# Kernel tuning notes

Measured on AMD Instinct MI355X. Metric: run time of the kernel, lower is better.

The kernel has to match this reference:

```python
import jax, jax.numpy as jnp
import numpy as np

B, L, D, H = 2, 2048, 1024, 16
DH = D // H
LN_EPS = 1e-5


def setup_inputs() -> dict:
    key = jax.random.key(0)
    ks = jax.random.split(key, 6)
    s = 1.0 / np.sqrt(D)
    return {
        "x": jax.random.normal(ks[0], (B, L, D), dtype=jnp.float32),
        "market_info": jax.random.uniform(ks[1], (B, 8), dtype=jnp.float32),
        "in_proj_w": jax.random.normal(ks[2], (3 * D, D), dtype=jnp.float32) * s,
        "in_proj_b": jnp.zeros((3 * D,), dtype=jnp.float32),
        "out_proj_w": jax.random.normal(ks[3], (D, D), dtype=jnp.float32) * s,
        "out_proj_b": jnp.zeros((D,), dtype=jnp.float32),
        "ln_gamma": jnp.ones((D,), dtype=jnp.float32),
        "ln_beta": jnp.zeros((D,), dtype=jnp.float32),
    }


def reference(x, market_info, in_proj_w, in_proj_b, out_proj_w, out_proj_b, ln_gamma, ln_beta):
    # fused QKV projection (torch nn.MultiheadAttention in_proj)
    qkv = jnp.einsum("bld,ed->ble", x, in_proj_w) + in_proj_b  # (B,L,3D)
    q, k, v = jnp.split(qkv, 3, axis=-1)
    q = q.reshape(B, L, H, DH)
    k = k.reshape(B, L, H, DH)
    v = v.reshape(B, L, H, DH)
    scale = 1.0 / jnp.sqrt(jnp.asarray(DH, dtype=x.dtype))
    scores = jnp.einsum("blhd,bmhd->bhlm", q, k) * scale  # (B,H,L,L)
    # market mask: per-batch volatility scalar added to every score
    vol = market_info[:, 0][:, None, None, None]  # (B,1,1,1)
    attn = jax.nn.softmax(scores + vol, axis=-1)
    ctx = jnp.einsum("bhlm,bmhd->blhd", attn, v).reshape(B, L, D)
    attended = jnp.einsum("bld,ed->ble", ctx, out_proj_w) + out_proj_b
    # residual + LayerNorm (dropout=0 / eval)
    y = x + attended
    mu = jnp.mean(y, axis=-1, keepdims=True)
    var = jnp.mean(jnp.square(y - mu), axis=-1, keepdims=True)
    return (y - mu) * jax.lax.rsqrt(var + LN_EPS) * ln_gamma + ln_beta
```

## Files before the change

### kernel.cpp

```cpp
#include <hip/hip_runtime.h>
#include <math.h>

#define B_  2
#define L_  2048
#define D_  1024
#define H_  16
#define DH_ 64
#define E3D 3072
#define LN_EPS 1e-5f

typedef unsigned short u16;
typedef __attribute__((ext_vector_type(8))) short bf16x8;
typedef __attribute__((ext_vector_type(4))) float f32x4;

__device__ inline unsigned pack2(float lo, float hi) {
    unsigned a = __builtin_bit_cast(unsigned, lo) + 0x8000u;
    unsigned b = __builtin_bit_cast(unsigned, hi) + 0x8000u;
    return __builtin_amdgcn_perm(b, a, 0x07060302);
}
__device__ inline float bf2f(u16 v) {
    return __builtin_bit_cast(float, (unsigned)v << 16);
}
__device__ inline void async16(const void* g, void* l) {
    __builtin_amdgcn_global_load_lds(
        (const __attribute__((address_space(1))) unsigned*)g,
        (__attribute__((address_space(3))) unsigned*)l, 16, 0, 0);
}

#define QSCALE (0.125f * 1.44269504088896f)

__global__ __launch_bounds__(256) void cvt_all(
    const float* __restrict__ x, const float* __restrict__ iw,
    const float* __restrict__ ow, u16* __restrict__ xb,
    u16* __restrict__ iwb, u16* __restrict__ owb)
{
    const int bid = blockIdx.x;
    const float* src; u16* dst; int base;
    if (bid < 2048)      { src = x;  dst = xb;  base = bid * 2048; }
    else if (bid < 3584) { src = iw; dst = iwb; base = (bid - 2048) * 2048; }
    else                 { src = ow; dst = owb; base = (bid - 3584) * 2048; }
    const int i = base + threadIdx.x * 8;
    float4 v0 = *(const float4*)(src + i);
    float4 v1 = *(const float4*)(src + i + 4);
    uint4 w;
    w.x = pack2(v0.x, v0.y); w.y = pack2(v0.z, v0.w);
    w.z = pack2(v1.x, v1.y); w.w = pack2(v1.z, v1.w);
    *(uint4*)(dst + i) = w;
}

template<int MT>
__global__ __launch_bounds__(256) void gemm_bf16(
    const u16* __restrict__ A, const u16* __restrict__ W,
    const float* __restrict__ bias, u16* __restrict__ outB,
    int M, int N, int K, int qlimit)
{
    constexpr int WC    = (MT == 128) ? 4 : 2;
    constexpr int SMEMB = (MT == 128) ? 34816 : 17408;
    __shared__ __align__(16) char smem[SMEMB];
    u16* As = (u16*)smem;
    u16* Ws = As + MT * 32;

    const int t    = threadIdx.x;
    const int wave = t >> 6;
    const int lane = t & 63;
    const int a    = lane & 15;
    const int g    = lane >> 4;
    const int row0 = blockIdx.y * MT;
    const int col0 = blockIdx.x * 128;

    const int srowA = wave * (MT / 4) + (lane >> 2);
    const int srowW = wave * 32 + (lane >> 2);
    const int sseg  = (lane & 3) * 8;
    const u16* Ag = A + (size_t)(row0 + srowA) * K + sseg;
    const u16* Wg = W + (size_t)(col0 + srowW) * K + sseg;
    u16* AsW = &As[wave * (MT / 4) * 32];
    u16* WsW = &Ws[wave * 32 * 32];

    f32x4 acc[4][WC];
    #pragma unroll
    for (int i = 0; i < 4; ++i)
        #pragma unroll
        for (int j = 0; j < WC; ++j)
            acc[i][j] = (f32x4){0.f, 0.f, 0.f, 0.f};

    const int ar = (MT == 128) ? (wave & 1) * 64 : 0;
    const int wc = (MT == 128) ? (wave >> 1) * 64 : wave * 32;

    for (int kt = 0; kt < K; kt += 32) {
        __syncthreads();
        if (MT == 128) {
            async16(Ag + kt,                  AsW);
            async16(Ag + (size_t)16 * K + kt, AsW + 16 * 32);
        } else {
            async16(Ag + kt, AsW);
        }
        async16(Wg + kt,                  WsW);
        async16(Wg + (size_t)16 * K + kt, WsW + 16 * 32);
        __syncthreads();

        bf16x8 af[4], wf[WC];
        #pragma unroll
        for (int i = 0; i < 4; ++i)
            af[i] = *(const bf16x8*)&As[(ar + i * 16 + a) * 32 + g * 8];
        #pragma unroll
        for (int j = 0; j < WC; ++j)
            wf[j] = *(const bf16x8*)&Ws[(wc + j * 16 + a) * 32 + g * 8];
        #pragma unroll
        for (int i = 0; i < 4; ++i)
            #pragma unroll
            for (int j = 0; j < WC; ++j)
                acc[i][j] = __builtin_amdgcn_mfma_f32_16x16x32_bf16(
                    wf[j], af[i], acc[i][j], 0, 0, 0);
    }

    const float s = (col0 < qlimit) ? QSCALE : 1.0f;
    __syncthreads();
    unsigned* Cs = (unsigned*)smem;
    #pragma unroll
    for (int j = 0; j < WC; ++j) {
        const int cb = wc + j * 16 + g * 4;
        const float4 bj = *(const float4*)(bias + col0 + cb);
        #pragma unroll
        for (int i = 0; i < 4; ++i) {
            const int row = ar + i * 16 + a;
            uint2 w;
            w.x = pack2((acc[i][j][0] + bj.x) * s, (acc[i][j][1] + bj.y) * s);
            w.y = pack2((acc[i][j][2] + bj.z) * s, (acc[i][j][3] + bj.w) * s);
            *(uint2*)&Cs[row * 68 + (cb >> 1)] = w;
        }
    }
    __syncthreads();
    #pragma unroll
    for (int p = 0; p < MT / 16; ++p) {
        const int rowX = (MT == 128) ? ((t >> 2) + (p & 1) * 64) : (t >> 2);
        const int c2X  = (MT == 128) ? ((t & 3) * 4 + (p >> 1) * 16)
                                     : ((t & 3) * 4 + p * 16);
        uint4 w = *(const uint4*)&Cs[rowX * 68 + c2X];
        *(uint4*)&outB[(size_t)(row0 + rowX) * N + col0 + c2X * 2] = w;
    }
}

__global__ __launch_bounds__(256) void attn_mfma(
    const u16* __restrict__ qkv, u16* __restrict__ Oun, float* __restrict__ lbuf)
{
    const int bid  = blockIdx.x;
    const int half = bid >> 9;
    const int rest = bid & 511;
    const int qt   = rest & 15;
    const int bh   = rest >> 4;
    const int h    = bh & 15;
    const int b    = bh >> 4;
    const int qb0  = qt * 128;

    const int t    = threadIdx.x;
    const int wave = t >> 6;
    const int lane = t & 63;
    const int a    = lane & 15;
    const int g    = lane >> 4;

    __shared__ __align__(16) u16 Kt[64 * 72];
    __shared__ __align__(16) u16 VtT[80 * 72];
    __shared__ __align__(16) u16 Pl[4 * 2 * 16 * 72];

    for (int idx = t; idx < 16 * 36; idx += 256) {
        const int r = idx / 36;
        const int w = idx - r * 36;
        ((unsigned*)VtT)[(64 + r) * 36 + w] = (r == 0) ? 0x3F803F80u : 0u;
    }

    bf16x8 qf[2][2];
    #pragma unroll
    for (int q2 = 0; q2 < 2; ++q2) {
        const u16* qrow = qkv + (size_t)(b * L_ + qb0 + wave * 32 + q2 * 16 + a) * E3D
                        + h * DH_;
        #pragma unroll
        for (int c = 0; c < 2; ++c)
            qf[q2][c] = *(const bf16x8*)(qrow + c * 32 + g * 8);
    }

    f32x4 o[2][4];
    f32x4 l4[2];
    #pragma unroll
    for (int q2 = 0; q2 < 2; ++q2) {
        #pragma unroll
        for (int dt = 0; dt < 4; ++dt)
            o[q2][dt] = (f32x4){0.f, 0.f, 0.f, 0.f};
        l4[q2] = (f32x4){0.f, 0.f, 0.f, 0.f};
    }

    const int krow = t >> 2;
    const int kseg = (t & 3) * 16;
    const int vu   = t >> 3;
    const int vc8  = (t & 7) * 8;
    const int vj0  = t & 7;

    const u16* kbase = qkv + (size_t)(b * L_) * E3D + D_ + h * DH_;
    const u16* vbase = qkv + (size_t)(b * L_) * E3D + 2 * D_ + h * DH_;

    const int k_lo = half * (L_ / 2);
    const int k_hi = k_lo + L_ / 2;

    uint4 kx0, kx1, va, vb;
    {
        const u16* kr = kbase + (size_t)(k_lo + krow) * E3D + kseg;
        kx0 = *(const uint4*)kr;
        kx1 = *(const uint4*)(kr + 8);
        const u16* vr = vbase + (size_t)(k_lo + 2 * vu) * E3D + vc8;
        va = *(const uint4*)vr;
        vb = *(const uint4*)(vr + E3D);
    }

    for (int k0 = k_lo; k0 < k_hi; k0 += 64) {
        __syncthreads();

        *(uint4*)&Kt[krow * 72 + kseg]     = kx0;
        *(uint4*)&Kt[krow * 72 + kseg + 8] = kx1;
        {
            const unsigned av[4] = {va.x, va.y, va.z, va.w};
            const unsigned bv[4] = {vb.x, vb.y, vb.z, vb.w};
            unsigned* Vw = (unsigned*)VtT;
            #pragma unroll
            for (int i = 0; i < 8; ++i) {
                const int j = (i + vj0) & 7;
                const unsigned xa = av[j >> 1], xb = bv[j >> 1];
                const unsigned v = (j & 1) ? ((xa >> 16) | (xb & 0xffff0000u))
                                           : ((xa & 0xffffu) | (xb << 16));
                Vw[(vc8 + j) * 36 + vu] = v;
            }
        }
        __syncthreads();

        if (k0 + 64 < k_hi) {
            const u16* kr = kbase + (size_t)(k0 + 64 + krow) * E3D + kseg;
            kx0 = *(const uint4*)kr;
            kx1 = *(const uint4*)(kr + 8);
            const u16* vr = vbase + (size_t)(k0 + 64 + 2 * vu) * E3D + vc8;
            va = *(const uint4*)vr;
            vb = *(const uint4*)(vr + E3D);
        }

        f32x4 s[2][4];
        #pragma unroll
        for (int q2 = 0; q2 < 2; ++q2)
            #pragma unroll
            for (int kt = 0; kt < 4; ++kt)
                s[q2][kt] = (f32x4){0.f, 0.f, 0.f, 0.f};
        #pragma unroll
        for (int kt = 0; kt < 4; ++kt) {
            bf16x8 kf0 = *(const bf16x8*)&Kt[(kt * 16 + a) * 72 + g * 8];
            bf16x8 kf1 = *(const bf16x8*)&Kt[(kt * 16 + a) * 72 + 32 + g * 8];
            #pragma unroll
            for (int q2 = 0; q2 < 2; ++q2) {
                s[q2][kt] = __builtin_amdgcn_mfma_f32_16x16x32_bf16(kf0, qf[q2][0], s[q2][kt], 0, 0, 0);
                s[q2][kt] = __builtin_amdgcn_mfma_f32_16x16x32_bf16(kf1, qf[q2][1], s[q2][kt], 0, 0, 0);
            }
        }

        #pragma unroll
        for (int q2 = 0; q2 < 2; ++q2) {
            unsigned* Pw = (unsigned*)&Pl[(wave * 2 + q2) * (16 * 72)];
            #pragma unroll
            for (int kt = 0; kt < 4; ++kt) {
                const float p0 = __builtin_amdgcn_exp2f(s[q2][kt][0]);
                const float p1 = __builtin_amdgcn_exp2f(s[q2][kt][1]);
                const float p2 = __builtin_amdgcn_exp2f(s[q2][kt][2]);
                const float p3 = __builtin_amdgcn_exp2f(s[q2][kt][3]);
                uint2 w;
                w.x = pack2(p0, p1);
                w.y = pack2(p2, p3);
                *(uint2*)&Pw[a * 36 + kt * 8 + g * 2] = w;
            }
        }

        #pragma unroll
        for (int c = 0; c < 2; ++c) {
            bf16x8 pf[2];
            #pragma unroll
            for (int q2 = 0; q2 < 2; ++q2)
                pf[q2] = *(const bf16x8*)&Pl[(wave * 2 + q2) * (16 * 72) + a * 72 + c * 32 + g * 8];
            #pragma unroll
            for (int dt = 0; dt < 4; ++dt) {
                bf16x8 vf = *(const bf16x8*)&VtT[(dt * 16 + a) * 72 + c * 32 + g * 8];
                #pragma unroll
                for (int q2 = 0; q2 < 2; ++q2)
                    o[q2][dt] = __builtin_amdgcn_mfma_f32_16x16x32_bf16(vf, pf[q2], o[q2][dt], 0, 0, 0);
            }
            {
                bf16x8 vf1 = *(const bf16x8*)&VtT[(64 + a) * 72 + c * 32 + g * 8];
                #pragma unroll
                for (int q2 = 0; q2 < 2; ++q2)
                    l4[q2] = __builtin_amdgcn_mfma_f32_16x16x32_bf16(vf1, pf[q2], l4[q2], 0, 0, 0);
            }
        }
    }

    #pragma unroll
    for (int q2 = 0; q2 < 2; ++q2) {
        const int qrow = qb0 + wave * 32 + q2 * 16 + a;
        const size_t row = (size_t)(b * L_ + qrow);
        if (g == 0)
            lbuf[(size_t)half * 65536 + row * 16 + h] = l4[q2][0];
        u16* cp = Oun + (size_t)half * 4096 * 1024 + row * D_ + h * DH_;
        #pragma unroll
        for (int dt = 0; dt < 4; ++dt) {
            uint2 w;
            w.x = pack2(o[q2][dt][0], o[q2][dt][1]);
            w.y = pack2(o[q2][dt][2], o[q2][dt][3]);
            *(uint2*)&cp[dt * 16 + g * 4] = w;
        }
    }
}

__global__ __launch_bounds__(256) void attn_merge(
    const u16* __restrict__ Oun, const float* __restrict__ lbuf,
    u16* __restrict__ ctx)
{
    const int row = blockIdx.x;
    const int t   = threadIdx.x;
    const int col = t * 4;
    const int h   = col >> 6;
    const float inv = 1.f / (lbuf[(size_t)row * 16 + h] +
                             lbuf[(size_t)65536 + row * 16 + h]);
    const size_t base = (size_t)row * D_ + col;
    uint2 w0 = *(const uint2*)&Oun[base];
    uint2 w1 = *(const uint2*)&Oun[(size_t)4096 * 1024 + base];
    float f0 = (bf2f((u16)(w0.x & 0xffff)) + bf2f((u16)(w1.x & 0xffff))) * inv;
    float f1 = (bf2f((u16)(w0.x >> 16))    + bf2f((u16)(w1.x >> 16)))    * inv;
    float f2 = (bf2f((u16)(w0.y & 0xffff)) + bf2f((u16)(w1.y & 0xffff))) * inv;
    float f3 = (bf2f((u16)(w0.y >> 16))    + bf2f((u16)(w1.y >> 16)))    * inv;
    uint2 w;
    w.x = pack2(f0, f1);
    w.y = pack2(f2, f3);
    *(uint2*)&ctx[base] = w;
}

__global__ __launch_bounds__(256) void ln_rows(
    const float* __restrict__ x, const u16* __restrict__ att,
    const float* __restrict__ gamma, const float* __restrict__ beta,
    float* __restrict__ out)
{
    const int row = blockIdx.x;
    const int t = threadIdx.x;
    const size_t base = (size_t)row * D_ + t * 4;

    float4 v = *(const float4*)(x + base);
    uint2 aw = *(const uint2*)(att + base);
    v.x += bf2f((u16)(aw.x & 0xffff));
    v.y += bf2f((u16)(aw.x >> 16));
    v.z += bf2f((u16)(aw.y & 0xffff));
    v.w += bf2f((u16)(aw.y >> 16));

    float s  = v.x + v.y + v.z + v.w;
    float s2 = v.x * v.x + v.y * v.y + v.z * v.z + v.w * v.w;
    #pragma unroll
    for (int off = 32; off > 0; off >>= 1) {
        s  += __shfl_down(s, off);
        s2 += __shfl_down(s2, off);
    }
    __shared__ float red[4], red2[4];
    const int wid = t >> 6, lid = t & 63;
    if (lid == 0) { red[wid] = s; red2[wid] = s2; }
    __syncthreads();
    if (t == 0) {
        float aa = 0.f, b2 = 0.f;
        #pragma unroll
        for (int i = 0; i < 4; ++i) { aa += red[i]; b2 += red2[i]; }
        red[0] = aa; red2[0] = b2;
    }
    __syncthreads();
    const float mu   = red[0] * (1.f / D_);
    const float var  = red2[0] * (1.f / D_) - mu * mu;
    const float rstd = rsqrtf(var + LN_EPS);

    float4 gm = *(const float4*)(gamma + t * 4);
    float4 bt = *(const float4*)(beta + t * 4);
    float4 oo;
    oo.x = (v.x - mu) * rstd * gm.x + bt.x;
    oo.y = (v.y - mu) * rstd * gm.y + bt.y;
    oo.z = (v.z - mu) * rstd * gm.z + bt.z;
    oo.w = (v.w - mu) * rstd * gm.w + bt.w;
    *(float4*)(out + base) = oo;
}

extern "C" void kernel_launch(void* const* d_in, const int* in_sizes, int n_in,
                              void* d_out, int out_size, void* d_ws, size_t ws_size,
                              hipStream_t stream)
{
    const float* x      = (const float*)d_in[0];
    const float* in_w   = (const float*)d_in[2];
    const float* in_b   = (const float*)d_in[3];
    const float* out_w  = (const float*)d_in[4];
    const float* out_b  = (const float*)d_in[5];
    const float* gamma  = (const float*)d_in[6];
    const float* beta   = (const float*)d_in[7];
    float* out = (float*)d_out;

    char* ws   = (char*)d_ws;
    u16*  qkvb = (u16*)ws;
    u16*  Oun  = (u16*)(ws + 25165824);
    u16*  po   = (u16*)(ws + 25165824);
    u16*  ctxb = (u16*)(ws + 41943040);
    u16*  xb   = (u16*)(ws + 50331648);
    float* lb  = (float*)(ws + 50331648);
    u16*  iwb  = (u16*)(ws + 58720256);
    u16*  owb  = (u16*)(ws + 65011712);

    dim3 blk(256);
    cvt_all<<<dim3(4096), blk, 0, stream>>>(x, in_w, out_w, xb, iwb, owb);

    gemm_bf16<128><<<dim3(E3D / 128, (B_ * L_) / 128), blk, 0, stream>>>(
        xb, iwb, in_b, qkvb, B_ * L_, E3D, D_, D_);

    attn_mfma<<<dim3(2 * B_ * H_ * (L_ / 128)), blk, 0, stream>>>(qkvb, Oun, lb);
    attn_merge<<<dim3(B_ * L_), blk, 0, stream>>>(Oun, lb, ctxb);

    gemm_bf16<64><<<dim3(D_ / 128, (B_ * L_) / 64), blk, 0, stream>>>(
        ctxb, owb, out_b, po, B_ * L_, D_, D_, 0);

    ln_rows<<<dim3(B_ * L_), blk, 0, stream>>>(x, po, gamma, beta, out);
}
```

Measured before the change: 221.6 us.

## Load K fragments directly from global into registers, bypassing LDS staging

```diff
diff --git a/kernel.cpp b/kernel.cpp
--- a/kernel.cpp
+++ b/kernel.cpp
@@ -158,7 +158,6 @@
     const int a    = lane & 15;
     const int g    = lane >> 4;
 
-    __shared__ __align__(16) u16 Kt[64 * 72];
     __shared__ __align__(16) u16 VtT[80 * 72];
     __shared__ __align__(16) u16 Pl[4 * 2 * 16 * 72];
 
@@ -178,6 +177,12 @@
             qf[q2][c] = *(const bf16x8*)(qrow + c * 32 + g * 8);
     }
 
+    __syncthreads();
+    bf16x8 onesf[2];
+    #pragma unroll
+    for (int c = 0; c < 2; ++c)
+        onesf[c] = *(const bf16x8*)&VtT[(64 + a) * 72 + c * 32 + g * 8];
+
     f32x4 o[2][4];
     f32x4 l4[2];
     #pragma unroll
@@ -188,33 +193,33 @@
         l4[q2] = (f32x4){0.f, 0.f, 0.f, 0.f};
     }
 
-    const int krow = t >> 2;
-    const int kseg = (t & 3) * 16;
     const int vu   = t >> 3;
     const int vc8  = (t & 7) * 8;
     const int vj0  = t & 7;
 
-    const u16* kbase = qkv + (size_t)(b * L_) * E3D + D_ + h * DH_;
+    const u16* kbase = qkv + (size_t)(b * L_) * E3D + D_ + h * DH_ + g * 8;
     const u16* vbase = qkv + (size_t)(b * L_) * E3D + 2 * D_ + h * DH_;
 
     const int k_lo = half * (L_ / 2);
     const int k_hi = k_lo + L_ / 2;
 
-    uint4 kx0, kx1, va, vb;
+    uint4 va, vb;
+    bf16x8 kf[4][2];
     {
-        const u16* kr = kbase + (size_t)(k_lo + krow) * E3D + kseg;
-        kx0 = *(const uint4*)kr;
-        kx1 = *(const uint4*)(kr + 8);
         const u16* vr = vbase + (size_t)(k_lo + 2 * vu) * E3D + vc8;
         va = *(const uint4*)vr;
         vb = *(const uint4*)(vr + E3D);
+        #pragma unroll
+        for (int kt = 0; kt < 4; ++kt) {
+            const u16* kp = kbase + (size_t)(k_lo + kt * 16 + a) * E3D;
+            kf[kt][0] = *(const bf16x8*)kp;
+            kf[kt][1] = *(const bf16x8*)(kp + 32);
+        }
     }
 
     for (int k0 = k_lo; k0 < k_hi; k0 += 64) {
         __syncthreads();
 
-        *(uint4*)&Kt[krow * 72 + kseg]     = kx0;
-        *(uint4*)&Kt[krow * 72 + kseg + 8] = kx1;
         {
             const unsigned av[4] = {va.x, va.y, va.z, va.w};
             const unsigned bv[4] = {vb.x, vb.y, vb.z, vb.w};
@@ -230,29 +235,29 @@
         }
         __syncthreads();
 
+        f32x4 s[2][4];
+        #pragma unroll
+        for (int q2 = 0; q2 < 2; ++q2)
+            #pragma unroll
+            for (int kt = 0; kt < 4; ++kt)
+                s[q2][kt] = (f32x4){0.f, 0.f, 0.f, 0.f};
+        #pragma unroll
+        for (int kt = 0; kt < 4; ++kt)
+            #pragma unroll
+            for (int q2 = 0; q2 < 2; ++q2) {
+                s[q2][kt] = __builtin_amdgcn_mfma_f32_16x16x32_bf16(kf[kt][0], qf[q2][0], s[q2][kt], 0, 0, 0);
+                s[q2][kt] = __builtin_amdgcn_mfma_f32_16x16x32_bf16(kf[kt][1], qf[q2][1], s[q2][kt], 0, 0, 0);
+            }
+
         if (k0 + 64 < k_hi) {
-            const u16* kr = kbase + (size_t)(k0 + 64 + krow) * E3D + kseg;
-            kx0 = *(const uint4*)kr;
-            kx1 = *(const uint4*)(kr + 8);
             const u16* vr = vbase + (size_t)(k0 + 64 + 2 * vu) * E3D + vc8;
             va = *(const uint4*)vr;
             vb = *(const uint4*)(vr + E3D);
-        }
-
-        f32x4 s[2][4];
-        #pragma unroll
-        for (int q2 = 0; q2 < 2; ++q2)
-            #pragma unroll
-            for (int kt = 0; kt < 4; ++kt)
-                s[q2][kt] = (f32x4){0.f, 0.f, 0.f, 0.f};
-        #pragma unroll
-        for (int kt = 0; kt < 4; ++kt) {
-            bf16x8 kf0 = *(const bf16x8*)&Kt[(kt * 16 + a) * 72 + g * 8];
-            bf16x8 kf1 = *(const bf16x8*)&Kt[(kt * 16 + a) * 72 + 32 + g * 8];
-            #pragma unroll
-            for (int q2 = 0; q2 < 2; ++q2) {
-                s[q2][kt] = __builtin_amdgcn_mfma_f32_16x16x32_bf16(kf0, qf[q2][0], s[q2][kt], 0, 0, 0);
-                s[q2][kt] = __builtin_amdgcn_mfma_f32_16x16x32_bf16(kf1, qf[q2][1], s[q2][kt], 0, 0, 0);
+            #pragma unroll
+            for (int kt = 0; kt < 4; ++kt) {
+                const u16* kp = kbase + (size_t)(k0 + 64 + kt * 16 + a) * E3D;
+                kf[kt][0] = *(const bf16x8*)kp;
+                kf[kt][1] = *(const bf16x8*)(kp + 32);
             }
         }
 
@@ -285,12 +290,9 @@
                 for (int q2 = 0; q2 < 2; ++q2)
                     o[q2][dt] = __builtin_amdgcn_mfma_f32_16x16x32_bf16(vf, pf[q2], o[q2][dt], 0, 0, 0);
             }
-            {
-                bf16x8 vf1 = *(const bf16x8*)&VtT[(64 + a) * 72 + c * 32 + g * 8];
-                #pragma unroll
-                for (int q2 = 0; q2 < 2; ++q2)
-                    l4[q2] = __builtin_amdgcn_mfma_f32_16x16x32_bf16(vf1, pf[q2], l4[q2], 0, 0, 0);
-            }
+            #pragma unroll
+            for (int q2 = 0; q2 < 2; ++q2)
+                l4[q2] = __builtin_amdgcn_mfma_f32_16x16x32_bf16(onesf[c], pf[q2], l4[q2], 0, 0, 0);
         }
     }
 
```

New measurement: 236.9 us. 1.07x slower.
